# Kernel optimization log

Measured on AMD Instinct MI355X. Metric: run time of the kernel, lower is better.

Reference implementation:

```python
import jax, jax.numpy as jnp
import numpy as np

# Inside algorithm for a binary TreeCRF over a complete binary tree in heap
# layout: node i has children 2i+1 and 2i+2; level of size n starts at index
# n-1. Leaves are the last (n_nodes+1)//2 entries of `emissions`.
#
# Original per-node math:
#   inside[p] = logsumexp_{i,j}( em[p] + trans[p,i] + left[i] + trans[p,j] + right[j] )
# which factorizes exactly as
#   inside[p] = em[p] + logsumexp_i(trans[p,i]+left[i]) + logsumexp_j(trans[p,j]+right[j])


def setup_inputs() -> dict:
    key = jax.random.key(0)
    k1, k2 = jax.random.split(key)
    n_leaves = 131072  # 2**17
    n_nodes = 2 * n_leaves - 1  # 262143
    L = 32
    emissions = jax.random.normal(k1, (n_nodes, L), dtype=jnp.float32)
    trans = jax.random.normal(k2, (L, L), dtype=jnp.float32)
    return {"emissions": emissions, "trans": trans}


def _child_contrib(trans, child):
    # child: [n, L] inside scores of children; trans: [L, L]
    # returns [n, L]: logsumexp_c(trans[p, c] + child[:, c])
    return jax.nn.logsumexp(trans[None, :, :] + child[:, None, :], axis=2)


def reference(emissions, trans):
    n_nodes = emissions.shape[0]
    n_leaves = (n_nodes + 1) // 2
    # leaf inside scores are just the leaf emissions
    scores = emissions[n_leaves - 1:]  # [n_leaves, L]
    level = n_leaves // 2
    while level >= 1:
        # children of node (level-1)+k are scores[2k] (left) and scores[2k+1] (right)
        left = scores[0::2]   # [level, L]
        right = scores[1::2]  # [level, L]
        em = emissions[level - 1: 2 * level - 1]  # [level, L]
        scores = em + _child_contrib(trans, left) + _child_contrib(trans, right)
        level //= 2
    return scores[0]  # root inside score, [L]
```

## Files before the change

kernel.cpp:

```cpp
#include <hip/hip_runtime.h>


typedef float f32x4 __attribute__((ext_vector_type(4)));
typedef short s16x8 __attribute__((ext_vector_type(8)));
typedef short s16x4 __attribute__((ext_vector_type(4)));

#define CSTR 40
#define LDS_WAIT() __asm__ volatile("s_waitcnt lgkmcnt(0)" ::: "memory")

__device__ __forceinline__ short f2bf(float f) {
    unsigned u = __builtin_bit_cast(unsigned, f);
    unsigned r = (u + 0x7fffu + ((u >> 16) & 1u)) >> 16;
    return (short)r;
}

__device__ __forceinline__ float max4(float4 v) {
    return fmaxf(fmaxf(v.x, v.y), fmaxf(v.z, v.w));
}

__device__ __forceinline__ void load_afrag(const float* __restrict__ trans,
                                           int row, int kg, s16x8* a)
{
#pragma unroll
    for (int j = 0; j < 8; ++j)
        (*a)[j] = f2bf(__expf(trans[row * 32 + kg * 8 + j]));
}

template <int NC0>
__device__ __forceinline__ void wave_reduce(
    int lane, const float* rows, const float* __restrict__ em, int inW,
    int sid, s16x8 a0, s16x8 a1, short* C, float* M, float* outrow)
{
    constexpr int STEPS = (NC0 == 32) ? 5 : 2;
    constexpr int NPH = (NC0 == 32) ? 6 : 2;
    const int ql = lane & 15, kg = lane >> 4;
    const int q0 = lane & 31, h = lane >> 5;

    float4 x0 = {0,0,0,0}, x1 = x0, x2 = x0, x3 = x0;
    if (q0 < NC0) {
        const float4* src = (const float4*)(rows + q0 * 32 + h * 16);
        x0 = src[0]; x1 = src[1]; x2 = src[2]; x3 = src[3];
    }

    float4 pe0[NPH], pe1[NPH];
    {
        int ph = 0;
#pragma unroll
        for (int s = 1; s <= STEPS; ++s) {
            const int nca = NC0 >> (s - 1);
            const int nstr = (nca >= 16) ? (nca >> 4) : 1;
#pragma unroll
            for (int st = 0; st < nstr; ++st, ++ph) {
                int p = (st * 16 + ql) >> 1;
                size_t node = (size_t)((inW >> s) - 1)
                            + (size_t)sid * (NC0 >> s) + p;
                pe0[ph] = *(const float4*)(em + node * 32 + kg * 4);
                pe1[ph] = *(const float4*)(em + node * 32 + 16 + kg * 4);
            }
        }
    }

    if (q0 < NC0) {
        float mm = fmaxf(fmaxf(max4(x0), max4(x1)),
                         fmaxf(max4(x2), max4(x3)));
        mm = fmaxf(mm, __shfl_xor(mm, 32));
        s16x8 w0, w1;
        w0[0] = f2bf(__expf(x0.x - mm)); w0[1] = f2bf(__expf(x0.y - mm));
        w0[2] = f2bf(__expf(x0.z - mm)); w0[3] = f2bf(__expf(x0.w - mm));
        w0[4] = f2bf(__expf(x1.x - mm)); w0[5] = f2bf(__expf(x1.y - mm));
        w0[6] = f2bf(__expf(x1.z - mm)); w0[7] = f2bf(__expf(x1.w - mm));
        w1[0] = f2bf(__expf(x2.x - mm)); w1[1] = f2bf(__expf(x2.y - mm));
        w1[2] = f2bf(__expf(x2.z - mm)); w1[3] = f2bf(__expf(x2.w - mm));
        w1[4] = f2bf(__expf(x3.x - mm)); w1[5] = f2bf(__expf(x3.y - mm));
        w1[6] = f2bf(__expf(x3.z - mm)); w1[7] = f2bf(__expf(x3.w - mm));
        *(s16x8*)(C + q0 * CSTR + h * 16) = w0;
        *(s16x8*)(C + q0 * CSTR + h * 16 + 8) = w1;
        if (h == 0) M[q0] = mm;
    }

    int nc = NC0, ph = 0;
#pragma unroll
    for (int s = 1; s <= STEPS; ++s) {
        const int nstr = (nc >= 16) ? (nc >> 4) : 1;
#pragma unroll
        for (int st = 0; st < nstr; ++st, ++ph) {
            LDS_WAIT();
            int q = st * 16 + ql;
            bool valid = q < nc;
            s16x8 b = *(const s16x8*)(C + q * CSTR + kg * 8);
            f32x4 d0 = {0.f, 0.f, 0.f, 0.f};
            f32x4 d1 = {0.f, 0.f, 0.f, 0.f};
            d0 = __builtin_amdgcn_mfma_f32_16x16x32_bf16(a0, b, d0, 0, 0, 0);
            d1 = __builtin_amdgcn_mfma_f32_16x16x32_bf16(a1, b, d1, 0, 0, 0);
            float mq = M[q];
            float mpair = mq + __shfl_xor(mq, 1);
            int p = q >> 1;
            float4 e0 = pe0[ph], e1 = pe1[ph];
            float w0[4] = {__expf(e0.x), __expf(e0.y),
                           __expf(e0.z), __expf(e0.w)};
            float w1[4] = {__expf(e1.x), __expf(e1.y),
                           __expf(e1.z), __expf(e1.w)};
            float u0[4], u1[4];
#pragma unroll
            for (int r = 0; r < 4; ++r) {
                u0[r] = d0[r] * __shfl_xor(d0[r], 1) * w0[r];
                u1[r] = d1[r] * __shfl_xor(d1[r], 1) * w1[r];
            }
            if (s == STEPS) {
                if (ql == 0) {
                    float4 o0 = {mpair + __logf(u0[0]), mpair + __logf(u0[1]),
                                 mpair + __logf(u0[2]), mpair + __logf(u0[3])};
                    float4 o1 = {mpair + __logf(u1[0]), mpair + __logf(u1[1]),
                                 mpair + __logf(u1[2]), mpair + __logf(u1[3])};
                    *(float4*)(outrow + kg * 4) = o0;
                    *(float4*)(outrow + 16 + kg * 4) = o1;
                }
            } else {
                float m2 = fmaxf(
                    fmaxf(fmaxf(u0[0], u0[1]), fmaxf(u0[2], u0[3])),
                    fmaxf(fmaxf(u1[0], u1[1]), fmaxf(u1[2], u1[3])));
                m2 = fmaxf(m2, __shfl_xor(m2, 16));
                m2 = fmaxf(m2, __shfl_xor(m2, 32));
                float inv = __fdividef(1.f, m2);
                if (valid && !(q & 1)) {
                    s16x4 z0, z1;
                    z0[0] = f2bf(u0[0] * inv); z0[1] = f2bf(u0[1] * inv);
                    z0[2] = f2bf(u0[2] * inv); z0[3] = f2bf(u0[3] * inv);
                    z1[0] = f2bf(u1[0] * inv); z1[1] = f2bf(u1[1] * inv);
                    z1[2] = f2bf(u1[2] * inv); z1[3] = f2bf(u1[3] * inv);
                    *(s16x4*)(C + p * CSTR + kg * 4) = z0;
                    *(s16x4*)(C + p * CSTR + 16 + kg * 4) = z1;
                    if (kg == 0) M[p] = mpair + __logf(m2);
                }
            }
        }
        nc >>= 1;
    }
}

__global__ __launch_bounds__(256) void treecrf_stage1(
    const float* __restrict__ rows_base, const float* __restrict__ em,
    const float* __restrict__ trans, float* __restrict__ out, int inW,
    int* __restrict__ counter)
{
    __shared__ short C[4 * 32 * CSTR];
    __shared__ float M[4 * 32];
    int t = threadIdx.x, lane = t & 63, wv = t >> 6;
    if (blockIdx.x == 0 && t == 0) *counter = 0;
    int sid = blockIdx.x * 4 + wv;
    s16x8 a0, a1;
    load_afrag(trans, lane & 15, lane >> 4, &a0);
    load_afrag(trans, (lane & 15) + 16, lane >> 4, &a1);
    wave_reduce<32>(lane, rows_base + (size_t)sid * 1024, em, inW, sid,
                    a0, a1, C + wv * 32 * CSTR, M + wv * 32,
                    out + (size_t)sid * 32);
}

__global__ __launch_bounds__(256) void treecrf_stage2(
    const float* __restrict__ ws1, float* __restrict__ ws2,
    const float* __restrict__ em, const float* __restrict__ trans,
    int* __restrict__ counter, float* __restrict__ out_root, int nbm1)
{
    __shared__ short C[4 * 32 * CSTR];
    __shared__ float M[4 * 32];
    __shared__ float R4[4 * 32];
    __shared__ int last_flag;
    int t = threadIdx.x, lane = t & 63, wv = t >> 6;
    int sid = blockIdx.x * 4 + wv;
    s16x8 a0, a1;
    load_afrag(trans, lane & 15, lane >> 4, &a0);
    load_afrag(trans, (lane & 15) + 16, lane >> 4, &a1);
    wave_reduce<32>(lane, ws1 + (size_t)sid * 1024, em, 4096, sid,
                    a0, a1, C + wv * 32 * CSTR, M + wv * 32,
                    ws2 + (size_t)sid * 32);

    if (t == 0) {
        __threadfence();
        last_flag = (atomicAdd(counter, 1) == nbm1);
    }
    __syncthreads();
    if (!last_flag) return;
    __threadfence();

    wave_reduce<32>(lane, ws2 + (size_t)wv * 1024, em, 128, wv,
                    a0, a1, C + wv * 32 * CSTR, M + wv * 32, R4 + wv * 32);
    __syncthreads();
    if (wv == 0)
        wave_reduce<4>(lane, R4, em, 4, 0, a0, a1, C, M, out_root);
}

extern "C" void kernel_launch(void* const* d_in, const int* in_sizes, int n_in,
                              void* d_out, int out_size, void* d_ws, size_t ws_size,
                              hipStream_t stream)
{
    const float* em = (const float*)d_in[0];
    const float* trans = (const float*)d_in[1];
    int n_nodes = in_sizes[0] / 32;
    int n_leaves = (n_nodes + 1) / 2;

    float* ws1 = (float*)d_ws;
    float* ws2 = ws1 + (size_t)4096 * 32;
    int* counter = (int*)(ws2 + (size_t)128 * 32);

    treecrf_stage1<<<dim3(n_leaves / 128), dim3(256), 0, stream>>>(
        em + (size_t)(n_leaves - 1) * 32, em, trans, ws1, n_leaves, counter);
    treecrf_stage2<<<dim3(32), dim3(256), 0, stream>>>(
        ws1, ws2, em, trans, counter, (float*)d_out, 31);
}
```

Measured before the change: 91.69 us.

## Fuse both tree-reduction stages into one kernel with per-block completion flags

Merges the two launches into a single kernel. The first 32 blocks spin-wait on completion flags from the 32 stage-1 blocks they depend on, and block 0 then waits on those 32 blocks to finish the root. This removes the second launch and its gap, and lets stage 2 start as soon as its inputs are ready. Per-level renormalisation now scales by a power of two taken from the exponent bits instead of a divide and a log. The cost is spin loops that rely on the waited-on blocks being scheduled, and flags that must be cleared at the end of each run.

```diff
diff --git a/kernel.cpp b/kernel.cpp
--- a/kernel.cpp
+++ b/kernel.cpp
@@ -7,6 +7,8 @@
 
 #define CSTR 40
 #define LDS_WAIT() __asm__ volatile("s_waitcnt lgkmcnt(0)" ::: "memory")
+#define DONE_MAGIC 0x5A17C0DE
+#define LN2F 0.69314718055994531f
 
 __device__ __forceinline__ short f2bf(float f) {
     unsigned u = __builtin_bit_cast(unsigned, f);
@@ -24,6 +26,19 @@
 #pragma unroll
     for (int j = 0; j < 8; ++j)
         (*a)[j] = f2bf(__expf(trans[row * 32 + kg * 8 + j]));
+}
+
+__device__ __forceinline__ void spin_acquire(int* flags, int lane, int n)
+{
+    bool got = lane >= n;
+    int idx = got ? 0 : lane;
+    for (;;) {
+        if (!got)
+            got = (atomicAdd(&flags[idx], 0) == DONE_MAGIC);
+        if (__all((int)got)) break;
+        __builtin_amdgcn_s_sleep(2);
+    }
+    __threadfence();
 }
 
 template <int NC0>
@@ -121,16 +136,19 @@
                     fmaxf(fmaxf(u1[0], u1[1]), fmaxf(u1[2], u1[3])));
                 m2 = fmaxf(m2, __shfl_xor(m2, 16));
                 m2 = fmaxf(m2, __shfl_xor(m2, 32));
-                float inv = __fdividef(1.f, m2);
+                unsigned mb = __builtin_bit_cast(unsigned, m2);
+                int ex = (int)((mb >> 23) & 0xFFu) - 127;
+                float scale = __builtin_bit_cast(float,
+                                                 (unsigned)(127 - ex) << 23);
                 if (valid && !(q & 1)) {
                     s16x4 z0, z1;
-                    z0[0] = f2bf(u0[0] * inv); z0[1] = f2bf(u0[1] * inv);
-                    z0[2] = f2bf(u0[2] * inv); z0[3] = f2bf(u0[3] * inv);
-                    z1[0] = f2bf(u1[0] * inv); z1[1] = f2bf(u1[1] * inv);
-                    z1[2] = f2bf(u1[2] * inv); z1[3] = f2bf(u1[3] * inv);
+                    z0[0] = f2bf(u0[0] * scale); z0[1] = f2bf(u0[1] * scale);
+                    z0[2] = f2bf(u0[2] * scale); z0[3] = f2bf(u0[3] * scale);
+                    z1[0] = f2bf(u1[0] * scale); z1[1] = f2bf(u1[1] * scale);
+                    z1[2] = f2bf(u1[2] * scale); z1[3] = f2bf(u1[3] * scale);
                     *(s16x4*)(C + p * CSTR + kg * 4) = z0;
                     *(s16x4*)(C + p * CSTR + 16 + kg * 4) = z1;
-                    if (kg == 0) M[p] = mpair + __logf(m2);
+                    if (kg == 0) M[p] = fmaf((float)ex, LN2F, mpair);
                 }
             }
         }
@@ -138,55 +156,47 @@
     }
 }
 
-__global__ __launch_bounds__(256) void treecrf_stage1(
-    const float* __restrict__ rows_base, const float* __restrict__ em,
-    const float* __restrict__ trans, float* __restrict__ out, int inW,
-    int* __restrict__ counter)
+__global__ __launch_bounds__(256) void treecrf_fused(
+    const float* __restrict__ em, const float* __restrict__ trans,
+    float* __restrict__ ws1, float* __restrict__ ws2,
+    int* __restrict__ f1, int* __restrict__ f2,
+    float* __restrict__ out_root, int n_leaves)
 {
     __shared__ short C[4 * 32 * CSTR];
     __shared__ float M[4 * 32];
+    __shared__ float R4[4 * 32];
     int t = threadIdx.x, lane = t & 63, wv = t >> 6;
-    if (blockIdx.x == 0 && t == 0) *counter = 0;
-    int sid = blockIdx.x * 4 + wv;
+    int b = blockIdx.x;
+    int sid = b * 4 + wv;
     s16x8 a0, a1;
     load_afrag(trans, lane & 15, lane >> 4, &a0);
     load_afrag(trans, (lane & 15) + 16, lane >> 4, &a1);
-    wave_reduce<32>(lane, rows_base + (size_t)sid * 1024, em, inW, sid,
-                    a0, a1, C + wv * 32 * CSTR, M + wv * 32,
-                    out + (size_t)sid * 32);
-}
-
-__global__ __launch_bounds__(256) void treecrf_stage2(
-    const float* __restrict__ ws1, float* __restrict__ ws2,
-    const float* __restrict__ em, const float* __restrict__ trans,
-    int* __restrict__ counter, float* __restrict__ out_root, int nbm1)
-{
-    __shared__ short C[4 * 32 * CSTR];
-    __shared__ float M[4 * 32];
-    __shared__ float R4[4 * 32];
-    __shared__ int last_flag;
-    int t = threadIdx.x, lane = t & 63, wv = t >> 6;
-    int sid = blockIdx.x * 4 + wv;
-    s16x8 a0, a1;
-    load_afrag(trans, lane & 15, lane >> 4, &a0);
-    load_afrag(trans, (lane & 15) + 16, lane >> 4, &a1);
+
+    wave_reduce<32>(lane, em + (size_t)(n_leaves - 1) * 32 + (size_t)sid * 1024,
+                    em, n_leaves, sid, a0, a1,
+                    C + wv * 32 * CSTR, M + wv * 32, ws1 + (size_t)sid * 32);
+    __syncthreads();
+    if (t == 0) { __threadfence(); atomicExch(&f1[b], DONE_MAGIC); }
+    if (b >= 32) return;
+
+    spin_acquire(f1 + b * 32 + wv * 8, lane, 8);
     wave_reduce<32>(lane, ws1 + (size_t)sid * 1024, em, 4096, sid,
                     a0, a1, C + wv * 32 * CSTR, M + wv * 32,
                     ws2 + (size_t)sid * 32);
-
-    if (t == 0) {
-        __threadfence();
-        last_flag = (atomicAdd(counter, 1) == nbm1);
-    }
     __syncthreads();
-    if (!last_flag) return;
-    __threadfence();
-
+    if (t == 0) { __threadfence(); atomicExch(&f2[b], DONE_MAGIC); }
+    if (b != 0) return;
+
+    spin_acquire(f2 + wv * 8, lane, 8);
     wave_reduce<32>(lane, ws2 + (size_t)wv * 1024, em, 128, wv,
                     a0, a1, C + wv * 32 * CSTR, M + wv * 32, R4 + wv * 32);
     __syncthreads();
-    if (wv == 0)
+    if (wv == 0) {
         wave_reduce<4>(lane, R4, em, 4, 0, a0, a1, C, M, out_root);
+    } else {
+        for (int i = t - 64; i < 1024; i += 192) f1[i] = 0;
+        if (t - 64 < 32) f2[t - 64] = 0;
+    }
 }
 
 extern "C" void kernel_launch(void* const* d_in, const int* in_sizes, int n_in,
@@ -200,10 +210,9 @@
 
     float* ws1 = (float*)d_ws;
     float* ws2 = ws1 + (size_t)4096 * 32;
-    int* counter = (int*)(ws2 + (size_t)128 * 32);
-
-    treecrf_stage1<<<dim3(n_leaves / 128), dim3(256), 0, stream>>>(
-        em + (size_t)(n_leaves - 1) * 32, em, trans, ws1, n_leaves, counter);
-    treecrf_stage2<<<dim3(32), dim3(256), 0, stream>>>(
-        ws1, ws2, em, trans, counter, (float*)d_out, 31);
-}
+    int* f1 = (int*)(ws2 + (size_t)128 * 32);
+    int* f2 = f1 + 1024;
+
+    treecrf_fused<<<dim3(n_leaves / 128), dim3(256), 0, stream>>>(
+        em, trans, ws1, ws2, f1, f2, (float*)d_out, n_leaves);
+}
```

Result: slower. 110.2 us (+20.2%).

## Process two subtrees per wave with interleaved MFMA chains and exponent rescaling

Applied to the files above, without the earlier changes.

Each wave now reduces two independent 32-row subtrees at once, interleaving their MFMA, shuffle and exp work so the serial per-level dependency chain has more instruction-level parallelism. Emission loads for the next level are prefetched one phase ahead instead of all up front, which lowers register pressure. Per-level renormalisation uses a power-of-two scale built from the max's exponent bits instead of a reciprocal and log. The grid is halved and launch bounds request two blocks per CU, which may reduce the number of waves available to hide latency.

```diff
diff --git a/kernel.cpp b/kernel.cpp
--- a/kernel.cpp
+++ b/kernel.cpp
@@ -7,6 +7,7 @@
 
 #define CSTR 40
 #define LDS_WAIT() __asm__ volatile("s_waitcnt lgkmcnt(0)" ::: "memory")
+#define LN2F 0.69314718055994531f
 
 __device__ __forceinline__ short f2bf(float f) {
     unsigned u = __builtin_bit_cast(unsigned, f);
@@ -26,13 +27,167 @@
         (*a)[j] = f2bf(__expf(trans[row * 32 + kg * 8 + j]));
 }
 
+__device__ __forceinline__ void stage0_tree(
+    int q0, int h, float4 x0, float4 x1, float4 x2, float4 x3,
+    short* Cp, float* Mp)
+{
+    float mm = fmaxf(fmaxf(max4(x0), max4(x1)), fmaxf(max4(x2), max4(x3)));
+    mm = fmaxf(mm, __shfl_xor(mm, 32));
+    s16x8 w0, w1;
+    w0[0] = f2bf(__expf(x0.x - mm)); w0[1] = f2bf(__expf(x0.y - mm));
+    w0[2] = f2bf(__expf(x0.z - mm)); w0[3] = f2bf(__expf(x0.w - mm));
+    w0[4] = f2bf(__expf(x1.x - mm)); w0[5] = f2bf(__expf(x1.y - mm));
+    w0[6] = f2bf(__expf(x1.z - mm)); w0[7] = f2bf(__expf(x1.w - mm));
+    w1[0] = f2bf(__expf(x2.x - mm)); w1[1] = f2bf(__expf(x2.y - mm));
+    w1[2] = f2bf(__expf(x2.z - mm)); w1[3] = f2bf(__expf(x2.w - mm));
+    w1[4] = f2bf(__expf(x3.x - mm)); w1[5] = f2bf(__expf(x3.y - mm));
+    w1[6] = f2bf(__expf(x3.z - mm)); w1[7] = f2bf(__expf(x3.w - mm));
+    *(s16x8*)(Cp + q0 * CSTR + h * 16) = w0;
+    *(s16x8*)(Cp + q0 * CSTR + h * 16 + 8) = w1;
+    if (h == 0) Mp[q0] = mm;
+}
+
+__device__ __forceinline__ void wave_reduce2(
+    int lane, const float* rowsA, const float* rowsB,
+    const float* __restrict__ em, int inW, int sidA, int sidB,
+    s16x8 a0, s16x8 a1, short* C, float* M, float* outA, float* outB)
+{
+    const int ql = lane & 15, kg = lane >> 4;
+    const int q0 = lane & 31, h = lane >> 5;
+    short* CB = C + 32 * CSTR;
+    float* MB = M + 32;
+
+    const float4* srcA = (const float4*)(rowsA + q0 * 32 + h * 16);
+    const float4* srcB = (const float4*)(rowsB + q0 * 32 + h * 16);
+    float4 xA0 = srcA[0], xA1 = srcA[1], xA2 = srcA[2], xA3 = srcA[3];
+    float4 xB0 = srcB[0], xB1 = srcB[1], xB2 = srcB[2], xB3 = srcB[3];
+
+    float4 eA0, eA1, eB0, eB1;
+    {
+        int p = ql >> 1;
+        size_t nA = (size_t)((inW >> 1) - 1) + (size_t)sidA * 16 + p;
+        size_t nB = (size_t)((inW >> 1) - 1) + (size_t)sidB * 16 + p;
+        eA0 = *(const float4*)(em + nA * 32 + kg * 4);
+        eA1 = *(const float4*)(em + nA * 32 + 16 + kg * 4);
+        eB0 = *(const float4*)(em + nB * 32 + kg * 4);
+        eB1 = *(const float4*)(em + nB * 32 + 16 + kg * 4);
+    }
+
+    stage0_tree(q0, h, xA0, xA1, xA2, xA3, C, M);
+    stage0_tree(q0, h, xB0, xB1, xB2, xB3, CB, MB);
+
+    constexpr int PS[6]  = {1, 1, 2, 3, 4, 5};
+    constexpr int PST[6] = {0, 1, 0, 0, 0, 0};
+    constexpr int PNC[6] = {32, 32, 16, 8, 4, 2};
+
+#pragma unroll
+    for (int ph = 0; ph < 6; ++ph) {
+        const int s = PS[ph], st = PST[ph], nc = PNC[ph];
+        float4 nA0, nA1, nB0, nB1;
+        if (ph < 5) {
+            const int s2 = PS[ph + 1], st2 = PST[ph + 1];
+            int p2 = (st2 * 16 + ql) >> 1;
+            size_t nA = (size_t)((inW >> s2) - 1)
+                      + (size_t)sidA * (32 >> s2) + p2;
+            size_t nB = (size_t)((inW >> s2) - 1)
+                      + (size_t)sidB * (32 >> s2) + p2;
+            nA0 = *(const float4*)(em + nA * 32 + kg * 4);
+            nA1 = *(const float4*)(em + nA * 32 + 16 + kg * 4);
+            nB0 = *(const float4*)(em + nB * 32 + kg * 4);
+            nB1 = *(const float4*)(em + nB * 32 + 16 + kg * 4);
+        }
+        LDS_WAIT();
+        const int q = st * 16 + ql;
+        const bool valid = q < nc;
+        s16x8 bA = *(const s16x8*)(C + q * CSTR + kg * 8);
+        s16x8 bB = *(const s16x8*)(CB + q * CSTR + kg * 8);
+        float mqA = M[q], mqB = MB[q];
+        f32x4 z = {0.f, 0.f, 0.f, 0.f};
+        f32x4 dA0 = __builtin_amdgcn_mfma_f32_16x16x32_bf16(a0, bA, z, 0, 0, 0);
+        f32x4 dA1 = __builtin_amdgcn_mfma_f32_16x16x32_bf16(a1, bA, z, 0, 0, 0);
+        f32x4 dB0 = __builtin_amdgcn_mfma_f32_16x16x32_bf16(a0, bB, z, 0, 0, 0);
+        f32x4 dB1 = __builtin_amdgcn_mfma_f32_16x16x32_bf16(a1, bB, z, 0, 0, 0);
+        float mpA = mqA + __shfl_xor(mqA, 1);
+        float mpB = mqB + __shfl_xor(mqB, 1);
+        float wA0[4] = {__expf(eA0.x), __expf(eA0.y),
+                        __expf(eA0.z), __expf(eA0.w)};
+        float wA1[4] = {__expf(eA1.x), __expf(eA1.y),
+                        __expf(eA1.z), __expf(eA1.w)};
+        float wB0[4] = {__expf(eB0.x), __expf(eB0.y),
+                        __expf(eB0.z), __expf(eB0.w)};
+        float wB1[4] = {__expf(eB1.x), __expf(eB1.y),
+                        __expf(eB1.z), __expf(eB1.w)};
+        float uA0[4], uA1[4], uB0[4], uB1[4];
+#pragma unroll
+        for (int r = 0; r < 4; ++r) {
+            uA0[r] = dA0[r] * __shfl_xor(dA0[r], 1) * wA0[r];
+            uA1[r] = dA1[r] * __shfl_xor(dA1[r], 1) * wA1[r];
+            uB0[r] = dB0[r] * __shfl_xor(dB0[r], 1) * wB0[r];
+            uB1[r] = dB1[r] * __shfl_xor(dB1[r], 1) * wB1[r];
+        }
+        if (ph == 5) {
+            if (ql == 0) {
+                float4 oA0 = {mpA + __logf(uA0[0]), mpA + __logf(uA0[1]),
+                              mpA + __logf(uA0[2]), mpA + __logf(uA0[3])};
+                float4 oA1 = {mpA + __logf(uA1[0]), mpA + __logf(uA1[1]),
+                              mpA + __logf(uA1[2]), mpA + __logf(uA1[3])};
+                float4 oB0 = {mpB + __logf(uB0[0]), mpB + __logf(uB0[1]),
+                              mpB + __logf(uB0[2]), mpB + __logf(uB0[3])};
+                float4 oB1 = {mpB + __logf(uB1[0]), mpB + __logf(uB1[1]),
+                              mpB + __logf(uB1[2]), mpB + __logf(uB1[3])};
+                *(float4*)(outA + kg * 4) = oA0;
+                *(float4*)(outA + 16 + kg * 4) = oA1;
+                *(float4*)(outB + kg * 4) = oB0;
+                *(float4*)(outB + 16 + kg * 4) = oB1;
+            }
+        } else {
+            float m2A = fmaxf(
+                fmaxf(fmaxf(uA0[0], uA0[1]), fmaxf(uA0[2], uA0[3])),
+                fmaxf(fmaxf(uA1[0], uA1[1]), fmaxf(uA1[2], uA1[3])));
+            m2A = fmaxf(m2A, __shfl_xor(m2A, 16));
+            m2A = fmaxf(m2A, __shfl_xor(m2A, 32));
+            float m2B = fmaxf(
+                fmaxf(fmaxf(uB0[0], uB0[1]), fmaxf(uB0[2], uB0[3])),
+                fmaxf(fmaxf(uB1[0], uB1[1]), fmaxf(uB1[2], uB1[3])));
+            m2B = fmaxf(m2B, __shfl_xor(m2B, 16));
+            m2B = fmaxf(m2B, __shfl_xor(m2B, 32));
+            unsigned mbA = __builtin_bit_cast(unsigned, m2A);
+            int exA = (int)((mbA >> 23) & 0xFFu) - 127;
+            float scA = __builtin_bit_cast(float, (unsigned)(127 - exA) << 23);
+            unsigned mbB = __builtin_bit_cast(unsigned, m2B);
+            int exB = (int)((mbB >> 23) & 0xFFu) - 127;
+            float scB = __builtin_bit_cast(float, (unsigned)(127 - exB) << 23);
+            int p = q >> 1;
+            if (valid && !(q & 1)) {
+                s16x4 zA0, zA1, zB0, zB1;
+                zA0[0] = f2bf(uA0[0] * scA); zA0[1] = f2bf(uA0[1] * scA);
+                zA0[2] = f2bf(uA0[2] * scA); zA0[3] = f2bf(uA0[3] * scA);
+                zA1[0] = f2bf(uA1[0] * scA); zA1[1] = f2bf(uA1[1] * scA);
+                zA1[2] = f2bf(uA1[2] * scA); zA1[3] = f2bf(uA1[3] * scA);
+                zB0[0] = f2bf(uB0[0] * scB); zB0[1] = f2bf(uB0[1] * scB);
+                zB0[2] = f2bf(uB0[2] * scB); zB0[3] = f2bf(uB0[3] * scB);
+                zB1[0] = f2bf(uB1[0] * scB); zB1[1] = f2bf(uB1[1] * scB);
+                zB1[2] = f2bf(uB1[2] * scB); zB1[3] = f2bf(uB1[3] * scB);
+                *(s16x4*)(C + p * CSTR + kg * 4) = zA0;
+                *(s16x4*)(C + p * CSTR + 16 + kg * 4) = zA1;
+                *(s16x4*)(CB + p * CSTR + kg * 4) = zB0;
+                *(s16x4*)(CB + p * CSTR + 16 + kg * 4) = zB1;
+                if (kg == 0) {
+                    M[p]  = fmaf((float)exA, LN2F, mpA);
+                    MB[p] = fmaf((float)exB, LN2F, mpB);
+                }
+            }
+            eA0 = nA0; eA1 = nA1; eB0 = nB0; eB1 = nB1;
+        }
+    }
+}
+
 template <int NC0>
 __device__ __forceinline__ void wave_reduce(
     int lane, const float* rows, const float* __restrict__ em, int inW,
     int sid, s16x8 a0, s16x8 a1, short* C, float* M, float* outrow)
 {
-    constexpr int STEPS = (NC0 == 32) ? 5 : 2;
-    constexpr int NPH = (NC0 == 32) ? 6 : 2;
+    constexpr int STEPS = 2, NPH = 2;
     const int ql = lane & 15, kg = lane >> 4;
     const int q0 = lane & 31, h = lane >> 5;
 
@@ -41,25 +196,14 @@
         const float4* src = (const float4*)(rows + q0 * 32 + h * 16);
         x0 = src[0]; x1 = src[1]; x2 = src[2]; x3 = src[3];
     }
-
     float4 pe0[NPH], pe1[NPH];
-    {
-        int ph = 0;
-#pragma unroll
-        for (int s = 1; s <= STEPS; ++s) {
-            const int nca = NC0 >> (s - 1);
-            const int nstr = (nca >= 16) ? (nca >> 4) : 1;
-#pragma unroll
-            for (int st = 0; st < nstr; ++st, ++ph) {
-                int p = (st * 16 + ql) >> 1;
-                size_t node = (size_t)((inW >> s) - 1)
-                            + (size_t)sid * (NC0 >> s) + p;
-                pe0[ph] = *(const float4*)(em + node * 32 + kg * 4);
-                pe1[ph] = *(const float4*)(em + node * 32 + 16 + kg * 4);
-            }
-        }
-    }
-
+#pragma unroll
+    for (int s = 1; s <= STEPS; ++s) {
+        int p = ql >> 1;
+        size_t node = (size_t)((inW >> s) - 1) + (size_t)sid * (NC0 >> s) + p;
+        pe0[s - 1] = *(const float4*)(em + node * 32 + kg * 4);
+        pe1[s - 1] = *(const float4*)(em + node * 32 + 16 + kg * 4);
+    }
     if (q0 < NC0) {
         float mm = fmaxf(fmaxf(max4(x0), max4(x1)),
                          fmaxf(max4(x2), max4(x3)));
@@ -77,102 +221,99 @@
         *(s16x8*)(C + q0 * CSTR + h * 16 + 8) = w1;
         if (h == 0) M[q0] = mm;
     }
-
-    int nc = NC0, ph = 0;
+    int nc = NC0;
 #pragma unroll
     for (int s = 1; s <= STEPS; ++s) {
-        const int nstr = (nc >= 16) ? (nc >> 4) : 1;
-#pragma unroll
-        for (int st = 0; st < nstr; ++st, ++ph) {
-            LDS_WAIT();
-            int q = st * 16 + ql;
-            bool valid = q < nc;
-            s16x8 b = *(const s16x8*)(C + q * CSTR + kg * 8);
-            f32x4 d0 = {0.f, 0.f, 0.f, 0.f};
-            f32x4 d1 = {0.f, 0.f, 0.f, 0.f};
-            d0 = __builtin_amdgcn_mfma_f32_16x16x32_bf16(a0, b, d0, 0, 0, 0);
-            d1 = __builtin_amdgcn_mfma_f32_16x16x32_bf16(a1, b, d1, 0, 0, 0);
-            float mq = M[q];
-            float mpair = mq + __shfl_xor(mq, 1);
-            int p = q >> 1;
-            float4 e0 = pe0[ph], e1 = pe1[ph];
-            float w0[4] = {__expf(e0.x), __expf(e0.y),
-                           __expf(e0.z), __expf(e0.w)};
-            float w1[4] = {__expf(e1.x), __expf(e1.y),
-                           __expf(e1.z), __expf(e1.w)};
-            float u0[4], u1[4];
-#pragma unroll
-            for (int r = 0; r < 4; ++r) {
-                u0[r] = d0[r] * __shfl_xor(d0[r], 1) * w0[r];
-                u1[r] = d1[r] * __shfl_xor(d1[r], 1) * w1[r];
+        LDS_WAIT();
+        int q = ql;
+        bool valid = q < nc;
+        s16x8 b = *(const s16x8*)(C + q * CSTR + kg * 8);
+        f32x4 zz = {0.f, 0.f, 0.f, 0.f};
+        f32x4 d0 = __builtin_amdgcn_mfma_f32_16x16x32_bf16(a0, b, zz, 0, 0, 0);
+        f32x4 d1 = __builtin_amdgcn_mfma_f32_16x16x32_bf16(a1, b, zz, 0, 0, 0);
+        float mq = M[q];
+        float mpair = mq + __shfl_xor(mq, 1);
+        int p = q >> 1;
+        float4 e0 = pe0[s - 1], e1 = pe1[s - 1];
+        float w0[4] = {__expf(e0.x), __expf(e0.y), __expf(e0.z), __expf(e0.w)};
+        float w1[4] = {__expf(e1.x), __expf(e1.y), __expf(e1.z), __expf(e1.w)};
+        float u0[4], u1[4];
+#pragma unroll
+        for (int r = 0; r < 4; ++r) {
+            u0[r] = d0[r] * __shfl_xor(d0[r], 1) * w0[r];
+            u1[r] = d1[r] * __shfl_xor(d1[r], 1) * w1[r];
+        }
+        if (s == STEPS) {
+            if (ql == 0) {
+                float4 o0 = {mpair + __logf(u0[0]), mpair + __logf(u0[1]),
+                             mpair + __logf(u0[2]), mpair + __logf(u0[3])};
+                float4 o1 = {mpair + __logf(u1[0]), mpair + __logf(u1[1]),
+                             mpair + __logf(u1[2]), mpair + __logf(u1[3])};
+                *(float4*)(outrow + kg * 4) = o0;
+                *(float4*)(outrow + 16 + kg * 4) = o1;
             }
-            if (s == STEPS) {
-                if (ql == 0) {
-                    float4 o0 = {mpair + __logf(u0[0]), mpair + __logf(u0[1]),
-                                 mpair + __logf(u0[2]), mpair + __logf(u0[3])};
-                    float4 o1 = {mpair + __logf(u1[0]), mpair + __logf(u1[1]),
-                                 mpair + __logf(u1[2]), mpair + __logf(u1[3])};
-                    *(float4*)(outrow + kg * 4) = o0;
-                    *(float4*)(outrow + 16 + kg * 4) = o1;
-                }
-            } else {
-                float m2 = fmaxf(
-                    fmaxf(fmaxf(u0[0], u0[1]), fmaxf(u0[2], u0[3])),
-                    fmaxf(fmaxf(u1[0], u1[1]), fmaxf(u1[2], u1[3])));
-                m2 = fmaxf(m2, __shfl_xor(m2, 16));
-                m2 = fmaxf(m2, __shfl_xor(m2, 32));
-                float inv = __fdividef(1.f, m2);
-                if (valid && !(q & 1)) {
-                    s16x4 z0, z1;
-                    z0[0] = f2bf(u0[0] * inv); z0[1] = f2bf(u0[1] * inv);
-                    z0[2] = f2bf(u0[2] * inv); z0[3] = f2bf(u0[3] * inv);
-                    z1[0] = f2bf(u1[0] * inv); z1[1] = f2bf(u1[1] * inv);
-                    z1[2] = f2bf(u1[2] * inv); z1[3] = f2bf(u1[3] * inv);
-                    *(s16x4*)(C + p * CSTR + kg * 4) = z0;
-                    *(s16x4*)(C + p * CSTR + 16 + kg * 4) = z1;
-                    if (kg == 0) M[p] = mpair + __logf(m2);
-                }
+        } else {
+            float m2 = fmaxf(
+                fmaxf(fmaxf(u0[0], u0[1]), fmaxf(u0[2], u0[3])),
+                fmaxf(fmaxf(u1[0], u1[1]), fmaxf(u1[2], u1[3])));
+            m2 = fmaxf(m2, __shfl_xor(m2, 16));
+            m2 = fmaxf(m2, __shfl_xor(m2, 32));
+            unsigned mb = __builtin_bit_cast(unsigned, m2);
+            int ex = (int)((mb >> 23) & 0xFFu) - 127;
+            float scale = __builtin_bit_cast(float, (unsigned)(127 - ex) << 23);
+            if (valid && !(q & 1)) {
+                s16x4 z0, z1;
+                z0[0] = f2bf(u0[0] * scale); z0[1] = f2bf(u0[1] * scale);
+                z0[2] = f2bf(u0[2] * scale); z0[3] = f2bf(u0[3] * scale);
+                z1[0] = f2bf(u1[0] * scale); z1[1] = f2bf(u1[1] * scale);
+                z1[2] = f2bf(u1[2] * scale); z1[3] = f2bf(u1[3] * scale);
+                *(s16x4*)(C + p * CSTR + kg * 4) = z0;
+                *(s16x4*)(C + p * CSTR + 16 + kg * 4) = z1;
+                if (kg == 0) M[p] = fmaf((float)ex, LN2F, mpair);
             }
         }
         nc >>= 1;
     }
 }
 
-__global__ __launch_bounds__(256) void treecrf_stage1(
+__global__ __launch_bounds__(256, 2) void treecrf_stage1(
     const float* __restrict__ rows_base, const float* __restrict__ em,
     const float* __restrict__ trans, float* __restrict__ out, int inW,
     int* __restrict__ counter)
 {
-    __shared__ short C[4 * 32 * CSTR];
-    __shared__ float M[4 * 32];
+    __shared__ short C[4 * 64 * CSTR];
+    __shared__ float M[4 * 64];
     int t = threadIdx.x, lane = t & 63, wv = t >> 6;
     if (blockIdx.x == 0 && t == 0) *counter = 0;
-    int sid = blockIdx.x * 4 + wv;
+    int w = blockIdx.x * 4 + wv;
+    int sidA = 2 * w, sidB = 2 * w + 1;
     s16x8 a0, a1;
     load_afrag(trans, lane & 15, lane >> 4, &a0);
     load_afrag(trans, (lane & 15) + 16, lane >> 4, &a1);
-    wave_reduce<32>(lane, rows_base + (size_t)sid * 1024, em, inW, sid,
-                    a0, a1, C + wv * 32 * CSTR, M + wv * 32,
-                    out + (size_t)sid * 32);
-}
-
-__global__ __launch_bounds__(256) void treecrf_stage2(
+    wave_reduce2(lane, rows_base + (size_t)sidA * 1024,
+                 rows_base + (size_t)sidB * 1024, em, inW, sidA, sidB,
+                 a0, a1, C + wv * 64 * CSTR, M + wv * 64,
+                 out + (size_t)sidA * 32, out + (size_t)sidB * 32);
+}
+
+__global__ __launch_bounds__(256, 2) void treecrf_stage2(
     const float* __restrict__ ws1, float* __restrict__ ws2,
     const float* __restrict__ em, const float* __restrict__ trans,
     int* __restrict__ counter, float* __restrict__ out_root, int nbm1)
 {
-    __shared__ short C[4 * 32 * CSTR];
-    __shared__ float M[4 * 32];
-    __shared__ float R4[4 * 32];
+    __shared__ short C[4 * 64 * CSTR];
+    __shared__ float M[4 * 64];
+    __shared__ float R4[128];
     __shared__ int last_flag;
     int t = threadIdx.x, lane = t & 63, wv = t >> 6;
-    int sid = blockIdx.x * 4 + wv;
+    int w = blockIdx.x * 4 + wv;
     s16x8 a0, a1;
     load_afrag(trans, lane & 15, lane >> 4, &a0);
     load_afrag(trans, (lane & 15) + 16, lane >> 4, &a1);
-    wave_reduce<32>(lane, ws1 + (size_t)sid * 1024, em, 4096, sid,
-                    a0, a1, C + wv * 32 * CSTR, M + wv * 32,
-                    ws2 + (size_t)sid * 32);
+    wave_reduce2(lane, ws1 + (size_t)(2 * w) * 1024,
+                 ws1 + (size_t)(2 * w + 1) * 1024, em, 4096, 2 * w, 2 * w + 1,
+                 a0, a1, C + wv * 64 * CSTR, M + wv * 64,
+                 ws2 + (size_t)(2 * w) * 32, ws2 + (size_t)(2 * w + 1) * 32);
 
     if (t == 0) {
         __threadfence();
@@ -182,8 +323,12 @@
     if (!last_flag) return;
     __threadfence();
 
-    wave_reduce<32>(lane, ws2 + (size_t)wv * 1024, em, 128, wv,
-                    a0, a1, C + wv * 32 * CSTR, M + wv * 32, R4 + wv * 32);
+    if (wv < 2)
+        wave_reduce2(lane, ws2 + (size_t)(2 * wv) * 1024,
+                     ws2 + (size_t)(2 * wv + 1) * 1024, em, 128,
+                     2 * wv, 2 * wv + 1,
+                     a0, a1, C + wv * 64 * CSTR, M + wv * 64,
+                     R4 + 2 * wv * 32, R4 + (2 * wv + 1) * 32);
     __syncthreads();
     if (wv == 0)
         wave_reduce<4>(lane, R4, em, 4, 0, a0, a1, C, M, out_root);
@@ -202,8 +347,8 @@
     float* ws2 = ws1 + (size_t)4096 * 32;
     int* counter = (int*)(ws2 + (size_t)128 * 32);
 
-    treecrf_stage1<<<dim3(n_leaves / 128), dim3(256), 0, stream>>>(
+    treecrf_stage1<<<dim3(n_leaves / 256), dim3(256), 0, stream>>>(
         em + (size_t)(n_leaves - 1) * 32, em, trans, ws1, n_leaves, counter);
-    treecrf_stage2<<<dim3(32), dim3(256), 0, stream>>>(
-        ws1, ws2, em, trans, counter, (float*)d_out, 31);
-}
+    treecrf_stage2<<<dim3(16), dim3(256), 0, stream>>>(
+        ws1, ws2, em, trans, counter, (float*)d_out, 15);
+}
```

New measurement: 94.71 us. 1.03x slower.
